# Optimization experiments

Measured on AMD Instinct MI355X. Metric: run time of the kernel, lower is better.

The kernel has to match this reference:

```python
import jax, jax.numpy as jnp
import numpy as np
import math

TIN = 4          # patch_size
NF = 128         # num_features
DM = 256         # d_model
NH = 8           # n_heads
HD = DM // NH    # head_dim = 32
FF = 1024        # ff_dim
NL = 4           # num_layers
MAXD = 64        # max_rel_dist -> L = 129


def _ln(x, g, b, eps):
    mu = jnp.mean(x, axis=-1, keepdims=True)
    var = jnp.mean(jnp.square(x - mu), axis=-1, keepdims=True)
    return (x - mu) * jax.lax.rsqrt(var + eps) * g + b


def setup_inputs() -> dict:
    key = jax.random.key(0)
    ks = jax.random.split(key, 24)
    s = 0.02
    d = {
        'x': jax.random.normal(ks[0], (2000, 16, NF), jnp.float32),
        'ln1_g': jnp.ones((TIN * NF,), jnp.float32),
        'ln1_b': jnp.zeros((TIN * NF,), jnp.float32),
        'proj_w': jax.random.normal(ks[1], (TIN * NF, DM), jnp.float32) * s,
        'proj_b': jnp.zeros((DM,), jnp.float32),
        'ln2_g': jnp.ones((DM,), jnp.float32),
        'ln2_b': jnp.zeros((DM,), jnp.float32),
        'rel_bias': jax.random.normal(ks[2], (NH, 2 * MAXD + 1), jnp.float32) * s,
        'ln_attn_g': jnp.ones((NL, DM), jnp.float32),
        'ln_attn_b': jnp.zeros((NL, DM), jnp.float32),
        'qkv_w': jax.random.normal(ks[3], (NL, DM, 3 * DM), jnp.float32) * s,
        'qkv_b': jnp.zeros((NL, 3 * DM), jnp.float32),
        'out_w': jax.random.normal(ks[4], (NL, DM, DM), jnp.float32) * s,
        'out_b': jnp.zeros((NL, DM), jnp.float32),
        'ln_ff_g': jnp.ones((NL, DM), jnp.float32),
        'ln_ff_b': jnp.zeros((NL, DM), jnp.float32),
        'ff1_w': jax.random.normal(ks[5], (NL, DM, FF), jnp.float32) * s,
        'ff1_b': jnp.zeros((NL, FF), jnp.float32),
        'ff2_w': jax.random.normal(ks[6], (NL, FF, DM), jnp.float32) * s,
        'ff2_b': jnp.zeros((NL, DM), jnp.float32),
        'fln_g': jnp.ones((DM,), jnp.float32),
        'fln_b': jnp.zeros((DM,), jnp.float32),
        'op_w': jax.random.normal(ks[7], (DM, NF), jnp.float32) * s,
        'op_b': jnp.zeros((NF,), jnp.float32),
    }
    return d


def reference(x, ln1_g, ln1_b, proj_w, proj_b, ln2_g, ln2_b, rel_bias,
              ln_attn_g, ln_attn_b, qkv_w, qkv_b, out_w, out_b,
              ln_ff_g, ln_ff_b, ff1_w, ff1_b, ff2_w, ff2_b,
              fln_g, fln_b, op_w, op_b):
    # ---- PatchEmbedding ----
    h = jnp.swapaxes(x, 0, 1)                 # [B, T, F]
    B, T, F = h.shape
    n_patch = T // TIN                        # 500 (== chunk_size, single chunk path)
    h = h[:, :n_patch * TIN, :].reshape(B, n_patch, TIN * F)
    h = _ln(h, ln1_g, ln1_b, 1e-6)
    h = h @ proj_w + proj_b
    h = _ln(h, ln2_g, ln2_b, 1e-6)            # [B, S, DM]
    S = n_patch

    # ---- relative position bias [H, S, S] ----
    pos = jnp.arange(S)
    rel = pos[None, :] - pos[:, None]
    idx = jnp.clip(rel, -MAXD, MAXD) + MAXD
    bias = rel_bias[:, idx]                   # [H, S, S]

    # ---- causal mask ----
    causal = jnp.triu(jnp.full((S, S), -jnp.inf, jnp.float32), k=1)
    scale = 1.0 / math.sqrt(HD)

    for l in range(NL):
        # attention block
        a = _ln(h, ln_attn_g[l], ln_attn_b[l], 1e-5)
        qkv = a @ qkv_w[l] + qkv_b[l]         # [B, S, 3*DM]
        q, k, v = jnp.split(qkv, 3, axis=-1)
        q = q.reshape(B, S, NH, HD)
        k = k.reshape(B, S, NH, HD)
        v = v.reshape(B, S, NH, HD)
        scores = jnp.einsum('bihd,bjhd->bhij', q, k) * scale
        scores = scores + bias[None] + causal
        attn = jax.nn.softmax(scores, axis=-1)
        o = jnp.einsum('bhij,bjhd->bihd', attn, v).reshape(B, S, DM)
        h = h + (o @ out_w[l] + out_b[l])
        # ffn block
        f = _ln(h, ln_ff_g[l], ln_ff_b[l], 1e-5)
        f = jax.nn.gelu(f @ ff1_w[l] + ff1_b[l], approximate=False)
        h = h + (f @ ff2_w[l] + ff2_b[l])

    h = _ln(h, fln_g, fln_b, 1e-5)
    h = h @ op_w + op_b                       # [B, S, NF]
    return jnp.swapaxes(h, 0, 1)              # [S, B, NF]
```

## Files before the change

### kernel.cpp

```cpp
#include <hip/hip_runtime.h>

#define TS 500
#define NB 16
#define NROW 8000
#define DMODEL 256
#define NHEAD 8
#define HDIM 32
#define FFD 1024

typedef __bf16 bf16x8 __attribute__((ext_vector_type(8)));
typedef __bf16 bf16x4 __attribute__((ext_vector_type(4)));
typedef float  f32x4  __attribute__((ext_vector_type(4)));
typedef float  f32x2  __attribute__((ext_vector_type(2)));

__device__ __forceinline__ float wred_sum(float v) {
    #pragma unroll
    for (int off = 32; off; off >>= 1) v += __shfl_xor(v, off, 64);
    return v;
}

__device__ __forceinline__ void pa_store(__bf16* __restrict__ PA, int KS,
                                         int grow, int col, float y) {
    int mt = grow >> 4, rl = grow & 15;
    size_t idx = ((size_t)(mt * KS + (col >> 5)) * 64 + ((col >> 3) & 3) * 16 + rl) * 8 + (col & 7);
// ... 33 lines not shown
    int k0 = ks * 32 + (lane >> 4) * 8;
    int col = nt * 16 + (lane & 15);
    const float* src = W + (size_t)l * wLS;
    bf16x8 v;
    #pragma unroll
    for (int j = 0; j < 8; j++) v[j] = (__bf16)src[(size_t)(k0 + j) * N + col];
    *(bf16x8*)(PB + (size_t)l * pLS + ((size_t)(nt * KS + ks) * 64 + lane) * 8) = v;
}

__global__ __launch_bounds__(256) void k_patchfused(
    const float* __restrict__ x, const float* __restrict__ g1, const float* __restrict__ b1,
    const __bf16* __restrict__ PBp, const float* __restrict__ bias,
    float* __restrict__ h,
    const float* __restrict__ gam, const float* __restrict__ bet,
    const float* __restrict__ gam2, const float* __restrict__ bet2,
    const __bf16* __restrict__ PBq0, const float* __restrict__ qb0,
    __bf16* __restrict__ qkvb)
{
    __shared__ __align__(16) __bf16 As[2][16][64][8];
    __shared__ float redS[4][32];
    __shared__ float redQ[4][32];
    int t = threadIdx.x, lane = t & 63, w = t >> 6;
    int row0 = blockIdx.x * 32;

    for (int rr = 0; rr < 8; rr++) {
        int lrow = w * 8 + rr;
        int row = row0 + lrow;
        int b = row / TS, pp = row - b * TS;
        int kb = lane * 8;
        const float* src = x + ((size_t)(pp * 4 + (kb >> 7)) * NB + b) * 128 + (kb & 127);
        float4 lo = *(const float4*)src;
        float4 hi = *(const float4*)(src + 4);
        float v[8] = {lo.x, lo.y, lo.z, lo.w, hi.x, hi.y, hi.z, hi.w};
        float sm_ = 0.f;
        #pragma unroll
        for (int j = 0; j < 8; j++) sm_ += v[j];
        sm_ = wred_sum(sm_);
        float mu = sm_ * (1.0f / 512.0f);
        float q = 0.f;
        #pragma unroll
        for (int j = 0; j < 8; j++) { float d = v[j] - mu; q += d * d; }
        q = wred_sum(q);
        float rs = rsqrtf(q * (1.0f / 512.0f) + 1e-6f);
        float4 gl = *(const float4*)(g1 + kb), gh = *(const float4*)(g1 + kb + 4);
        float4 bl = *(const float4*)(b1 + kb), bh = *(const float4*)(b1 + kb + 4);
        float gg[8] = {gl.x, gl.y, gl.z, gl.w, gh.x, gh.y, gh.z, gh.w};
        float bbv[8] = {bl.x, bl.y, bl.z, bl.w, bh.x, bh.y, bh.z, bh.w};
        bf16x8 yv;
        #pragma unroll
        for (int j = 0; j < 8; j++) yv[j] = (__bf16)((v[j] - mu) * rs * gg[j] + bbv[j]);
        *(bf16x8*)&As[lrow >> 4][lane >> 2][(lane & 3) * 16 + (lrow & 15)][0] = yv;
    }
    __syncthreads();

    const bf16x8* B8 = (const bf16x8*)PBp;
    f32x4 acc[2][4] = {};
    #pragma unroll 8
    for (int ks = 0; ks < 16; ks++) {
        bf16x8 a0 = *(const bf16x8*)&As[0][ks][lane][0];
        bf16x8 a1 = *(const bf16x8*)&As[1][ks][lane][0];
        #pragma unroll
        for (int n = 0; n < 4; n++) {
            bf16x8 b = B8[((size_t)(w * 4 + n) * 16 + ks) * 64 + lane];
            acc[0][n] = __builtin_amdgcn_mfma_f32_16x16x32_bf16(a0, b, acc[0][n], 0, 0, 0);
            acc[1][n] = __builtin_amdgcn_mfma_f32_16x16x32_bf16(a1, b, acc[1][n], 0, 0, 0);
        }
    }

    int g_ = lane >> 4, cl = lane & 15;
    int rbase = g_ * 4;
    float gamv[4], betv[4], gam2v[4], bet2v[4];
    #pragma unroll
    for (int n = 0; n < 4; n++) {
        int col = (w * 4 + n) * 16 + cl;
        float bv = bias[col];
        gamv[n] = gam[col]; betv[n] = bet[col];
        gam2v[n] = gam2[col]; bet2v[n] = bet2[col];
        #pragma unroll
        for (int m = 0; m < 2; m++)
            #pragma unroll
            for (int r = 0; r < 4; r++) acc[m][n][r] += bv;
    }
    float mu[2][4], rstd[2][4];
    {
        float ps[2][4];
        #pragma unroll
        for (int m = 0; m < 2; m++)
            #pragma unroll
            for (int r = 0; r < 4; r++) {
                float s2 = acc[m][0][r] + acc[m][1][r] + acc[m][2][r] + acc[m][3][r];
                #pragma unroll
                for (int off = 1; off < 16; off <<= 1) s2 += __shfl_xor(s2, off, 64);
                ps[m][r] = s2;
            }
        if (cl == 0)
            #pragma unroll
            for (int m = 0; m < 2; m++)
                #pragma unroll
                for (int r = 0; r < 4; r++) redS[w][m * 16 + rbase + r] = ps[m][r];
        __syncthreads();
        #pragma unroll
        for (int m = 0; m < 2; m++)
            #pragma unroll
            for (int r = 0; r < 4; r++) {
                int lr = m * 16 + rbase + r;
                mu[m][r] = (redS[0][lr] + redS[1][lr] + redS[2][lr] + redS[3][lr]) * (1.0f / 256.0f);
            }
        float pq[2][4];
        #pragma unroll
        for (int m = 0; m < 2; m++)
            #pragma unroll
            for (int r = 0; r < 4; r++) {
                float s2 = 0.f;
                #pragma unroll
                for (int n = 0; n < 4; n++) { float d = acc[m][n][r] - mu[m][r]; s2 += d * d; }
                #pragma unroll
                for (int off = 1; off < 16; off <<= 1) s2 += __shfl_xor(s2, off, 64);
                pq[m][r] = s2;
            }
        if (cl == 0)
            #pragma unroll
            for (int m = 0; m < 2; m++)
                #pragma unroll
                for (int r = 0; r < 4; r++) redQ[w][m * 16 + rbase + r] = pq[m][r];
        __syncthreads();
        #pragma unroll
        for (int m = 0; m < 2; m++)
            #pragma unroll
            for (int r = 0; r < 4; r++) {
                int lr = m * 16 + rbase + r;
                float var = (redQ[0][lr] + redQ[1][lr] + redQ[2][lr] + redQ[3][lr]) * (1.0f / 256.0f);
                rstd[m][r] = rsqrtf(var + 1e-6f);
            }
    }
    float ps2[2][4];
    #pragma unroll
    for (int m = 0; m < 2; m++) {
        int row = row0 + m * 16 + rbase;
        #pragma unroll
        for (int r = 0; r < 4; r++) {
            float s2 = 0.f;
            #pragma unroll
            for (int n = 0; n < 4; n++) {
                int col = (w * 4 + n) * 16 + cl;
                float y1 = (acc[m][n][r] - mu[m][r]) * rstd[m][r] * gamv[n] + betv[n];
                h[(size_t)(row + r) * 256 + col] = y1;
                s2 += y1;
            }
            #pragma unroll
            for (int off = 1; off < 16; off <<= 1) s2 += __shfl_xor(s2, off, 64);
            ps2[m][r] = s2;
        }
    }
    if (cl == 0)
        #pragma unroll
        for (int m = 0; m < 2; m++)
            #pragma unroll
            for (int r = 0; r < 4; r++) redS[w][m * 16 + rbase + r] = ps2[m][r];
    __syncthreads();
    float mu2[2][4], rstd2[2][4];
    #pragma unroll
    for (int m = 0; m < 2; m++)
        #pragma unroll
        for (int r = 0; r < 4; r++) {
            int lr = m * 16 + rbase + r;
            mu2[m][r] = (redS[0][lr] + redS[1][lr] + redS[2][lr] + redS[3][lr]) * (1.0f / 256.0f);
        }
    float pq2[2][4];
    #pragma unroll
    for (int m = 0; m < 2; m++)
        #pragma unroll
        for (int r = 0; r < 4; r++) {
            float s2 = 0.f;
            #pragma unroll
            for (int n = 0; n < 4; n++) {
                float y1 = (acc[m][n][r] - mu[m][r]) * rstd[m][r] * gamv[n] + betv[n];
                float d = y1 - mu2[m][r];
                s2 += d * d;
            }
            #pragma unroll
            for (int off = 1; off < 16; off <<= 1) s2 += __shfl_xor(s2, off, 64);
            pq2[m][r] = s2;
        }
    if (cl == 0)
        #pragma unroll
        for (int m = 0; m < 2; m++)
            #pragma unroll
            for (int r = 0; r < 4; r++) redQ[w][m * 16 + rbase + r] = pq2[m][r];
    __syncthreads();
    #pragma unroll
    for (int m = 0; m < 2; m++)
        #pragma unroll
        for (int r = 0; r < 4; r++) {
            int lr = m * 16 + rbase + r;
            float var = (redQ[0][lr] + redQ[1][lr] + redQ[2][lr] + redQ[3][lr]) * (1.0f / 256.0f);
            rstd2[m][r] = rsqrtf(var + 1e-5f);
        }
    __bf16* YA = &As[0][0][0][0];
    #pragma unroll
    for (int m = 0; m < 2; m++) {
        #pragma unroll
        for (int n = 0; n < 4; n++) {
            int col = (w * 4 + n) * 16 + cl;
            #pragma unroll
            for (int r = 0; r < 4; r++) {
                float y1 = (acc[m][n][r] - mu[m][r]) * rstd[m][r] * gamv[n] + betv[n];
                float y2 = (y1 - mu2[m][r]) * rstd2[m][r] * gam2v[n] + bet2v[n];
                ya_store(YA, m * 16 + rbase + r, col, y2);
            }
        }
    }
    __syncthreads();

    const bf16x8* YA8 = (const bf16x8*)YA;
    const bf16x8* B8q = (const bf16x8*)PBq0;
    for (int m = 0; m < 2; m++) {
        f32x4 acc2[12] = {};
        for (int ks = 0; ks < 8; ks++) {
            bf16x8 a = YA8[(m * 8 + ks) * 64 + lane];
            #pragma unroll
            for (int n = 0; n < 12; n++) {
                bf16x8 b = B8q[((size_t)(w * 12 + n) * 8 + ks) * 64 + lane];
                acc2[n] = __builtin_amdgcn_mfma_f32_16x16x32_bf16(a, b, acc2[n], 0, 0, 0);
            }
        }
        int row = row0 + m * 16 + rbase;
        #pragma unroll
        for (int n = 0; n < 12; n++) {
            int col = (w * 12 + n) * 16 + cl;
            float bv = qb0[col];
            #pragma unroll
            for (int r = 0; r < 4; r++)
                qkvb[(size_t)(row + r) * 768 + col] = (__bf16)(acc2[n][r] + bv);
        }
    }
}

template<int MODE>
__global__ __launch_bounds__(512) void k_layer(
    const __bf16* __restrict__ PAattn, const __bf16* __restrict__ PBo,
    const float* __restrict__ ob, float* __restrict__ h,
    const float* __restrict__ fg, const float* __restrict__ fb,
    const __bf16* __restrict__ PB1, const float* __restrict__ b1,
    const __bf16* __restrict__ PB2, const float* __restrict__ b2,
    const float* __restrict__ gam, const float* __restrict__ bet,
    const __bf16* __restrict__ PBn, const float* __restrict__ bn,
    __bf16* __restrict__ qkvb, float* __restrict__ outp)
{
    __shared__ __align__(16) __bf16 YA[8 * 64 * 8];
    __shared__ __align__(16) __bf16 F1T[1024][16];
    __shared__ float redS[8][16];
    __shared__ float redQ[8][16];
    int t = threadIdx.x, lane = t & 63, w = t >> 6;
    int mt = blockIdx.x;
    int g_ = lane >> 4, cl = lane & 15, rbase = g_ * 4;
    int row = mt * 16 + rbase;

    const bf16x8* A8 = (const bf16x8*)PAattn;
    const bf16x8* B8o = (const bf16x8*)PBo;
    const bf16x8* B81 = (const bf16x8*)PB1;
    const bf16x8* B82 = (const bf16x8*)PB2;

    f32x4 hv[2] = {};
    {
        f32x4 acc0[2] = {};
        #pragma unroll 8
        for (int ks = 0; ks < 8; ks++) {
            bf16x8 a = A8[((size_t)mt * 8 + ks) * 64 + lane];
            #pragma unroll
            for (int n = 0; n < 2; n++) {
                bf16x8 b = B8o[((size_t)(w * 2 + n) * 8 + ks) * 64 + lane];
                acc0[n] = __builtin_amdgcn_mfma_f32_16x16x32_bf16(a, b, acc0[n], 0, 0, 0);
            }
        }
        #pragma unroll
        for (int n = 0; n < 2; n++) {
            int col = (w * 2 + n) * 16 + cl;
            float bv = ob[col];
            #pragma unroll
            for (int r = 0; r < 4; r++)
                hv[n][r] = acc0[n][r] + bv + h[(size_t)(row + r) * 256 + col];
        }
    }
    {
        float mu[4], rstd[4];
        float ps[4];
        #pragma unroll
        for (int r = 0; r < 4; r++) {
            float s2 = hv[0][r] + hv[1][r];
            #pragma unroll
            for (int off = 1; off < 16; off <<= 1) s2 += __shfl_xor(s2, off, 64);
            ps[r] = s2;
        }
        if (cl == 0)
            #pragma unroll
            for (int r = 0; r < 4; r++) redS[w][rbase + r] = ps[r];
        __syncthreads();
        #pragma unroll
        for (int r = 0; r < 4; r++) {
            int lr = rbase + r;
            float s2 = 0.f;
            #pragma unroll
            for (int ww = 0; ww < 8; ww++) s2 += redS[ww][lr];
            mu[r] = s2 * (1.0f / 256.0f);
        }
        float pq[4];
        #pragma unroll
        for (int r = 0; r < 4; r++) {
            float s2 = 0.f;
            #pragma unroll
            for (int n = 0; n < 2; n++) { float d = hv[n][r] - mu[r]; s2 += d * d; }
            #pragma unroll
            for (int off = 1; off < 16; off <<= 1) s2 += __shfl_xor(s2, off, 64);
            pq[r] = s2;
        }
        if (cl == 0)
            #pragma unroll
            for (int r = 0; r < 4; r++) redQ[w][rbase + r] = pq[r];
        __syncthreads();
        #pragma unroll
        for (int r = 0; r < 4; r++) {
            int lr = rbase + r;
            float s2 = 0.f;
            #pragma unroll
            for (int ww = 0; ww < 8; ww++) s2 += redQ[ww][lr];
            rstd[r] = rsqrtf(s2 * (1.0f / 256.0f) + 1e-5f);
        }
        #pragma unroll
        for (int n = 0; n < 2; n++) {
            int col = (w * 2 + n) * 16 + cl;
            float gv = fg[col], bv = fb[col];
            #pragma unroll
            for (int r = 0; r < 4; r++) {
                float y = (hv[n][r] - mu[r]) * rstd[r] * gv + bv;
                ya_store(YA, rbase + r, col, y);
            }
        }
    }
    __syncthreads();

    const bf16x8* YA8 = (const bf16x8*)YA;
    {
        f32x4 acc1[8] = {};
        #pragma unroll 2
        for (int ks = 0; ks < 8; ks++) {
            bf16x8 a = YA8[ks * 64 + lane];
            #pragma unroll
            for (int n = 0; n < 8; n++) {
                bf16x8 b = B81[((size_t)(w * 8 + n) * 8 + ks) * 64 + lane];
                acc1[n] = __builtin_amdgcn_mfma_f32_16x16x32_bf16(a, b, acc1[n], 0, 0, 0);
            }
        }
        #pragma unroll
        for (int n = 0; n < 8; n++) {
            int col = (w * 8 + n) * 16 + cl;
            float bv = b1[col];
            bf16x4 pv;
            #pragma unroll
            for (int r = 0; r < 4; r++) {
                float xx = acc1[n][r] + bv;
                pv[r] = (__bf16)(0.5f * xx * (1.0f + erff(xx * 0.70710678118654752f)));
            }
            *(bf16x4*)&F1T[col][rbase] = pv;
        }
    }
    __syncthreads();

    f32x4 acc[2] = {};
    for (int kb = 0; kb < 8; kb++) {
        f32x2 lo[4], hi[4];
        #pragma unroll
        for (int q = 0; q < 4; q++) {
            unsigned ta = (unsigned)(uintptr_t)&F1T[(kb * 4 + q) * 32 + 8 * g_][0] + cl * 8;
            asm volatile("ds_read_b64_tr_b16 %0, %1" : "=v"(lo[q]) : "v"(ta) : "memory");
            asm volatile("ds_read_b64_tr_b16 %0, %1 offset:128" : "=v"(hi[q]) : "v"(ta) : "memory");
        }
        asm volatile("s_waitcnt lgkmcnt(0)" ::: "memory");
        __builtin_amdgcn_sched_barrier(0);
        #pragma unroll
        for (int q = 0; q < 4; q++) {
            int ks = kb * 4 + q;
            f32x4 pc = {lo[q][0], lo[q][1], hi[q][0], hi[q][1]};
            bf16x8 a = __builtin_bit_cast(bf16x8, pc);
            #pragma unroll
            for (int n = 0; n < 2; n++) {
                bf16x8 b = B82[((size_t)(w * 2 + n) * 32 + ks) * 64 + lane];
                acc[n] = __builtin_amdgcn_mfma_f32_16x16x32_bf16(a, b, acc[n], 0, 0, 0);
            }
        }
    }

    float gamv[2], betv[2];
    #pragma unroll
    for (int n = 0; n < 2; n++) {
        int col = (w * 2 + n) * 16 + cl;
        float bv = b2[col];
        gamv[n] = gam[col]; betv[n] = bet[col];
        #pragma unroll
        for (int r = 0; r < 4; r++) {
            float v = acc[n][r] + bv + hv[n][r];
            h[(size_t)(row + r) * 256 + col] = v;
            acc[n][r] = v;
        }
    }
    {
        float mu[4], rstd[4];
        float ps[4];
        #pragma unroll
        for (int r = 0; r < 4; r++) {
            float s2 = acc[0][r] + acc[1][r];
            #pragma unroll
            for (int off = 1; off < 16; off <<= 1) s2 += __shfl_xor(s2, off, 64);
            ps[r] = s2;
        }
        if (cl == 0)
            #pragma unroll
            for (int r = 0; r < 4; r++) redS[w][rbase + r] = ps[r];
        __syncthreads();
        #pragma unroll
        for (int r = 0; r < 4; r++) {
            int lr = rbase + r;
            float s2 = 0.f;
            #pragma unroll
            for (int ww = 0; ww < 8; ww++) s2 += redS[ww][lr];
            mu[r] = s2 * (1.0f / 256.0f);
        }
        float pq[4];
        #pragma unroll
        for (int r = 0; r < 4; r++) {
            float s2 = 0.f;
            #pragma unroll
            for (int n = 0; n < 2; n++) { float d = acc[n][r] - mu[r]; s2 += d * d; }
            #pragma unroll
            for (int off = 1; off < 16; off <<= 1) s2 += __shfl_xor(s2, off, 64);
            pq[r] = s2;
        }
        if (cl == 0)
            #pragma unroll
            for (int r = 0; r < 4; r++) redQ[w][rbase + r] = pq[r];
        __syncthreads();
        #pragma unroll
        for (int r = 0; r < 4; r++) {
            int lr = rbase + r;
            float s2 = 0.f;
            #pragma unroll
            for (int ww = 0; ww < 8; ww++) s2 += redQ[ww][lr];
            rstd[r] = rsqrtf(s2 * (1.0f / 256.0f) + 1e-5f);
        }
        #pragma unroll
        for (int n = 0; n < 2; n++) {
            int col = (w * 2 + n) * 16 + cl;
            #pragma unroll
            for (int r = 0; r < 4; r++) {
                float y = (acc[n][r] - mu[r]) * rstd[r] * gamv[n] + betv[n];
                ya_store(YA, rbase + r, col, y);
            }
        }
    }
    __syncthreads();

    const bf16x8* B8n = (const bf16x8*)PBn;
    if constexpr (MODE == 0) {
        f32x4 acc2[6] = {};
        for (int ks = 0; ks < 8; ks++) {
            bf16x8 a = YA8[ks * 64 + lane];
            #pragma unroll
            for (int n = 0; n < 6; n++) {
                bf16x8 b = B8n[((size_t)(w * 6 + n) * 8 + ks) * 64 + lane];
                acc2[n] = __builtin_amdgcn_mfma_f32_16x16x32_bf16(a, b, acc2[n], 0, 0, 0);
            }
        }
        #pragma unroll
        for (int n = 0; n < 6; n++) {
            int col = (w * 6 + n) * 16 + cl;
            float bv = bn[col];
            #pragma unroll
            for (int r = 0; r < 4; r++)
                qkvb[(size_t)(row + r) * 768 + col] = (__bf16)(acc2[n][r] + bv);
        }
    } else {
        f32x4 acc2 = {};
        #pragma unroll 4
        for (int ks = 0; ks < 8; ks++) {
            bf16x8 a = YA8[ks * 64 + lane];
            bf16x8 b = B8n[((size_t)w * 8 + ks) * 64 + lane];
            acc2 = __builtin_amdgcn_mfma_f32_16x16x32_bf16(a, b, acc2, 0, 0, 0);
        }
        int col = w * 16 + cl;
        float bv = bn[col];
        #pragma unroll
        for (int r = 0; r < 4; r++) {
            int grow = row + r;
            int bq = grow / TS, pp = grow - bq * TS;
            outp[((size_t)pp * NB + bq) * 128 + col] = acc2[r] + bv;
        }
    }
}

__global__ __launch_bounds__(512) void k_attn(
    const __bf16* __restrict__ qkv, const float* __restrict__ rel_bias,
    __bf16* __restrict__ PA)
{
    __shared__ __align__(16) __bf16 Kfr[4][64][8];
    __shared__ __align__(16) __bf16 Vpl[2][64][16];
    __shared__ __align__(16) __bf16 PT[8][64][16];
    __shared__ float bias_s[132];

    int bh = blockIdx.x;
    int pr = 3 - blockIdx.y;
    int b = bh >> 3, hh = bh & 7;
    int t = threadIdx.x, lane = t & 63, w = t >> 6;
    int wg = w & 3, grp = w >> 2;
    int qt = 2 * pr + 1 - grp;
    int q0 = qt * 64 + wg * 16;
    int c = lane & 15, g = lane >> 4;

    const __bf16* base = qkv + (size_t)b * TS * 768 + hh * 32;

    if (t < 129) bias_s[t] = rel_bias[hh * 129 + t];

    bf16x8 aq = {};
    {
        int qi = q0 + c;
        if (qi < TS) aq = *(const bf16x8*)(base + (size_t)qi * 768 + 8 * g);
    }

    float lpart[4] = {0.f, 0.f, 0.f, 0.f};
// ... 125 lines not shown
    const float* ln_ff_b  = (const float*)d_in[15];
    const float* ff1_w    = (const float*)d_in[16];
    const float* ff1_b    = (const float*)d_in[17];
    const float* ff2_w    = (const float*)d_in[18];
    const float* ff2_b    = (const float*)d_in[19];
    const float* fln_g    = (const float*)d_in[20];
    const float* fln_b    = (const float*)d_in[21];
    const float* op_w     = (const float*)d_in[22];
    const float* op_b     = (const float*)d_in[23];
    float* out = (float*)d_out;

    char* ws = (char*)d_ws;
    float*  h     = (float*)(ws);
    __bf16* qkvb  = (__bf16*)(ws + 8192000);
    __bf16* PA    = (__bf16*)(ws + 20480000);
    __bf16* PBq   = (__bf16*)(ws + 24576000);
    __bf16* PBo   = (__bf16*)(ws + 26148864);
    __bf16* PB1   = (__bf16*)(ws + 26673152);
    __bf16* PB2   = (__bf16*)(ws + 28770304);
    __bf16* PBp   = (__bf16*)(ws + 30867456);
    __bf16* PBop  = (__bf16*)(ws + 31129600);

    k_pack_all<<<1616, 256, 0, stream>>>(qkv_w, out_w, ff1_w, ff2_w, proj_w, op_w,
                                         PBq, PBo, PB1, PB2, PBp, PBop);

    k_patchfused<<<250, 256, 0, stream>>>(x, ln1_g, ln1_b, PBp, proj_b, h,
                                          ln2_g, ln2_b, ln_attn_g, ln_attn_b,
                                          PBq, qkv_b, qkvb);

    for (int l = 0; l < 4; l++) {
        dim3 ag(NB * NHEAD, 4);
        k_attn<<<ag, 512, 0, stream>>>(qkvb, rel_bias, PA);
        if (l < 3) {
            k_layer<0><<<500, 512, 0, stream>>>(PA, PBo + (size_t)l * 65536, out_b + l * 256,
                                                h, ln_ff_g + l * 256, ln_ff_b + l * 256,
                                                PB1 + (size_t)l * 262144, ff1_b + l * 1024,
                                                PB2 + (size_t)l * 262144, ff2_b + l * 256,
                                                ln_attn_g + (l + 1) * 256, ln_attn_b + (l + 1) * 256,
                                                PBq + (size_t)(l + 1) * 196608, qkv_b + (l + 1) * 768,
                                                qkvb, nullptr);
        } else {
            k_layer<1><<<500, 512, 0, stream>>>(PA, PBo + (size_t)l * 65536, out_b + l * 256,
                                                h, ln_ff_g + l * 256, ln_ff_b + l * 256,
                                                PB1 + (size_t)l * 262144, ff1_b + l * 1024,
                                                PB2 + (size_t)l * 262144, ff2_b + l * 256,
                                                fln_g, fln_b,
                                                PBop, op_b, nullptr, out);
        }
    }
}
```

Measured before the change: 283.7 us.

## Process two 16-row M tiles per layer block to reuse weight loads

Each k_layer block now handles 32 rows (two 16-row MFMA tiles) instead of 16, so every B-weight fragment loaded from global memory feeds two MFMAs. The FF1/FF2 stage is split into two halves of 512 columns so the transposed F1T buffer stays the same size in LDS. The grid is halved from 500 to 250 blocks. This cuts weight traffic per row but reduces parallelism below the CU count, raises register pressure, and adds extra barriers.

```diff
diff --git a/kernel.cpp b/kernel.cpp
--- a/kernel.cpp
+++ b/kernel.cpp
@@ -304,30 +304,31 @@
     const __bf16* __restrict__ PBn, const float* __restrict__ bn,
     __bf16* __restrict__ qkvb, float* __restrict__ outp)
 {
-    __shared__ __align__(16) __bf16 YA[8 * 64 * 8];
-    __shared__ __align__(16) __bf16 F1T[1024][16];
-    __shared__ float redS[8][16];
-    __shared__ float redQ[8][16];
+    __shared__ __align__(16) __bf16 YA[2 * 8 * 64 * 8];
+    __shared__ __align__(16) __bf16 F1T[2][512][16];
+    __shared__ float redS[8][32];
+    __shared__ float redQ[8][32];
     int t = threadIdx.x, lane = t & 63, w = t >> 6;
-    int mt = blockIdx.x;
+    int mt0 = blockIdx.x * 2;
     int g_ = lane >> 4, cl = lane & 15, rbase = g_ * 4;
-    int row = mt * 16 + rbase;
 
     const bf16x8* A8 = (const bf16x8*)PAattn;
     const bf16x8* B8o = (const bf16x8*)PBo;
     const bf16x8* B81 = (const bf16x8*)PB1;
     const bf16x8* B82 = (const bf16x8*)PB2;
 
-    f32x4 hv[2] = {};
+    f32x4 hv[2][2];
     {
-        f32x4 acc0[2] = {};
+        f32x4 acc0[2][2] = {};
         #pragma unroll 8
         for (int ks = 0; ks < 8; ks++) {
-            bf16x8 a = A8[((size_t)mt * 8 + ks) * 64 + lane];
+            bf16x8 a0 = A8[((size_t)mt0 * 8 + ks) * 64 + lane];
+            bf16x8 a1 = A8[((size_t)(mt0 + 1) * 8 + ks) * 64 + lane];
             #pragma unroll
             for (int n = 0; n < 2; n++) {
                 bf16x8 b = B8o[((size_t)(w * 2 + n) * 8 + ks) * 64 + lane];
-                acc0[n] = __builtin_amdgcn_mfma_f32_16x16x32_bf16(a, b, acc0[n], 0, 0, 0);
+                acc0[0][n] = __builtin_amdgcn_mfma_f32_16x16x32_bf16(a0, b, acc0[0][n], 0, 0, 0);
+                acc0[1][n] = __builtin_amdgcn_mfma_f32_16x16x32_bf16(a1, b, acc0[1][n], 0, 0, 0);
             }
         }
         #pragma unroll
@@ -335,116 +336,152 @@
             int col = (w * 2 + n) * 16 + cl;
             float bv = ob[col];
             #pragma unroll
-            for (int r = 0; r < 4; r++)
-                hv[n][r] = acc0[n][r] + bv + h[(size_t)(row + r) * 256 + col];
+            for (int m = 0; m < 2; m++) {
+                int row = (mt0 + m) * 16 + rbase;
+                #pragma unroll
+                for (int r = 0; r < 4; r++)
+                    hv[m][n][r] = acc0[m][n][r] + bv + h[(size_t)(row + r) * 256 + col];
+            }
         }
     }
     {
-        float mu[4], rstd[4];
-        float ps[4];
-        #pragma unroll
-        for (int r = 0; r < 4; r++) {
-            float s2 = hv[0][r] + hv[1][r];
-            #pragma unroll
-            for (int off = 1; off < 16; off <<= 1) s2 += __shfl_xor(s2, off, 64);
-            ps[r] = s2;
-        }
+        float mu[2][4], rstd[2][4];
+        float ps[2][4];
+        #pragma unroll
+        for (int m = 0; m < 2; m++)
+            #pragma unroll
+            for (int r = 0; r < 4; r++) {
+                float s2 = hv[m][0][r] + hv[m][1][r];
+                #pragma unroll
+                for (int off = 1; off < 16; off <<= 1) s2 += __shfl_xor(s2, off, 64);
+                ps[m][r] = s2;
+            }
         if (cl == 0)
             #pragma unroll
-            for (int r = 0; r < 4; r++) redS[w][rbase + r] = ps[r];
-        __syncthreads();
-        #pragma unroll
-        for (int r = 0; r < 4; r++) {
-            int lr = rbase + r;
-            float s2 = 0.f;
-            #pragma unroll
-            for (int ww = 0; ww < 8; ww++) s2 += redS[ww][lr];
-            mu[r] = s2 * (1.0f / 256.0f);
-        }
-        float pq[4];
-        #pragma unroll
-        for (int r = 0; r < 4; r++) {
-            float s2 = 0.f;
-            #pragma unroll
-            for (int n = 0; n < 2; n++) { float d = hv[n][r] - mu[r]; s2 += d * d; }
-            #pragma unroll
-            for (int off = 1; off < 16; off <<= 1) s2 += __shfl_xor(s2, off, 64);
-            pq[r] = s2;
-        }
+            for (int m = 0; m < 2; m++)
+                #pragma unroll
+                for (int r = 0; r < 4; r++) redS[w][m * 16 + rbase + r] = ps[m][r];
+        __syncthreads();
+        #pragma unroll
+        for (int m = 0; m < 2; m++)
+            #pragma unroll
+            for (int r = 0; r < 4; r++) {
+                int lr = m * 16 + rbase + r;
+                float s2 = 0.f;
+                #pragma unroll
+                for (int ww = 0; ww < 8; ww++) s2 += redS[ww][lr];
+                mu[m][r] = s2 * (1.0f / 256.0f);
+            }
+        float pq[2][4];
+        #pragma unroll
+        for (int m = 0; m < 2; m++)
+            #pragma unroll
+            for (int r = 0; r < 4; r++) {
+                float s2 = 0.f;
+                #pragma unroll
+                for (int n = 0; n < 2; n++) { float d = hv[m][n][r] - mu[m][r]; s2 += d * d; }
+                #pragma unroll
+                for (int off = 1; off < 16; off <<= 1) s2 += __shfl_xor(s2, off, 64);
+                pq[m][r] = s2;
+            }
         if (cl == 0)
             #pragma unroll
-            for (int r = 0; r < 4; r++) redQ[w][rbase + r] = pq[r];
-        __syncthreads();
-        #pragma unroll
-        for (int r = 0; r < 4; r++) {
-            int lr = rbase + r;
-            float s2 = 0.f;
-            #pragma unroll
-            for (int ww = 0; ww < 8; ww++) s2 += redQ[ww][lr];
-            rstd[r] = rsqrtf(s2 * (1.0f / 256.0f) + 1e-5f);
-        }
+            for (int m = 0; m < 2; m++)
+                #pragma unroll
+                for (int r = 0; r < 4; r++) redQ[w][m * 16 + rbase + r] = pq[m][r];
+        __syncthreads();
+        #pragma unroll
+        for (int m = 0; m < 2; m++)
+            #pragma unroll
+            for (int r = 0; r < 4; r++) {
+                int lr = m * 16 + rbase + r;
+                float s2 = 0.f;
+                #pragma unroll
+                for (int ww = 0; ww < 8; ww++) s2 += redQ[ww][lr];
+                rstd[m][r] = rsqrtf(s2 * (1.0f / 256.0f) + 1e-5f);
+            }
         #pragma unroll
         for (int n = 0; n < 2; n++) {
             int col = (w * 2 + n) * 16 + cl;
             float gv = fg[col], bv = fb[col];
             #pragma unroll
-            for (int r = 0; r < 4; r++) {
-                float y = (hv[n][r] - mu[r]) * rstd[r] * gv + bv;
-                ya_store(YA, rbase + r, col, y);
-            }
+            for (int m = 0; m < 2; m++)
+                #pragma unroll
+                for (int r = 0; r < 4; r++) {
+                    float y = (hv[m][n][r] - mu[m][r]) * rstd[m][r] * gv + bv;
+                    ya_store(YA, m * 16 + rbase + r, col, y);
+                }
         }
     }
     __syncthreads();
 
     const bf16x8* YA8 = (const bf16x8*)YA;
-    {
-        f32x4 acc1[8] = {};
-        #pragma unroll 2
-        for (int ks = 0; ks < 8; ks++) {
-            bf16x8 a = YA8[ks * 64 + lane];
-            #pragma unroll
-            for (int n = 0; n < 8; n++) {
-                bf16x8 b = B81[((size_t)(w * 8 + n) * 8 + ks) * 64 + lane];
-                acc1[n] = __builtin_amdgcn_mfma_f32_16x16x32_bf16(a, b, acc1[n], 0, 0, 0);
-            }
-        }
-        #pragma unroll
-        for (int n = 0; n < 8; n++) {
-            int col = (w * 8 + n) * 16 + cl;
-            float bv = b1[col];
-            bf16x4 pv;
-            #pragma unroll
-            for (int r = 0; r < 4; r++) {
-                float xx = acc1[n][r] + bv;
-                pv[r] = (__bf16)(0.5f * xx * (1.0f + erff(xx * 0.70710678118654752f)));
-            }
-            *(bf16x4*)&F1T[col][rbase] = pv;
-        }
-    }
-    __syncthreads();
-
-    f32x4 acc[2] = {};
-    for (int kb = 0; kb < 8; kb++) {
-        f32x2 lo[4], hi[4];
-        #pragma unroll
-        for (int q = 0; q < 4; q++) {
-            unsigned ta = (unsigned)(uintptr_t)&F1T[(kb * 4 + q) * 32 + 8 * g_][0] + cl * 8;
-            asm volatile("ds_read_b64_tr_b16 %0, %1" : "=v"(lo[q]) : "v"(ta) : "memory");
-            asm volatile("ds_read_b64_tr_b16 %0, %1 offset:128" : "=v"(hi[q]) : "v"(ta) : "memory");
-        }
-        asm volatile("s_waitcnt lgkmcnt(0)" ::: "memory");
-        __builtin_amdgcn_sched_barrier(0);
-        #pragma unroll
-        for (int q = 0; q < 4; q++) {
-            int ks = kb * 4 + q;
-            f32x4 pc = {lo[q][0], lo[q][1], hi[q][0], hi[q][1]};
-            bf16x8 a = __builtin_bit_cast(bf16x8, pc);
-            #pragma unroll
-            for (int n = 0; n < 2; n++) {
-                bf16x8 b = B82[((size_t)(w * 2 + n) * 32 + ks) * 64 + lane];
-                acc[n] = __builtin_amdgcn_mfma_f32_16x16x32_bf16(a, b, acc[n], 0, 0, 0);
-            }
-        }
+    f32x4 acc[2][2] = {};
+    #pragma unroll
+    for (int hf = 0; hf < 2; hf++) {
+        {
+            f32x4 acc1[2][4] = {};
+            #pragma unroll 2
+            for (int ks = 0; ks < 8; ks++) {
+                bf16x8 a0 = YA8[ks * 64 + lane];
+                bf16x8 a1 = YA8[(8 + ks) * 64 + lane];
+                #pragma unroll
+                for (int n = 0; n < 4; n++) {
+                    int nt = hf * 32 + w * 4 + n;
+                    bf16x8 b = B81[((size_t)nt * 8 + ks) * 64 + lane];
+                    acc1[0][n] = __builtin_amdgcn_mfma_f32_16x16x32_bf16(a0, b, acc1[0][n], 0, 0, 0);
+                    acc1[1][n] = __builtin_amdgcn_mfma_f32_16x16x32_bf16(a1, b, acc1[1][n], 0, 0, 0);
+                }
+            }
+            #pragma unroll
+            for (int n = 0; n < 4; n++) {
+                int colh = (w * 4 + n) * 16 + cl;
+                float bv = b1[hf * 512 + colh];
+                #pragma unroll
+                for (int m = 0; m < 2; m++) {
+                    bf16x4 pv;
+                    #pragma unroll
+                    for (int r = 0; r < 4; r++) {
+                        float xx = acc1[m][n][r] + bv;
+                        pv[r] = (__bf16)(0.5f * xx * (1.0f + erff(xx * 0.70710678118654752f)));
+                    }
+                    *(bf16x4*)&F1T[m][colh][rbase] = pv;
+                }
+            }
+        }
+        __syncthreads();
+
+        for (int kb = 0; kb < 4; kb++) {
+            f32x2 lo[2][4], hi[2][4];
+            #pragma unroll
+            for (int q = 0; q < 4; q++) {
+                #pragma unroll
+                for (int m = 0; m < 2; m++) {
+                    unsigned ta = (unsigned)(uintptr_t)&F1T[m][(kb * 4 + q) * 32 + 8 * g_][0] + cl * 8;
+                    asm volatile("ds_read_b64_tr_b16 %0, %1" : "=v"(lo[m][q]) : "v"(ta) : "memory");
+                    asm volatile("ds_read_b64_tr_b16 %0, %1 offset:128" : "=v"(hi[m][q]) : "v"(ta) : "memory");
+                }
+            }
+            asm volatile("s_waitcnt lgkmcnt(0)" ::: "memory");
+            __builtin_amdgcn_sched_barrier(0);
+            #pragma unroll
+            for (int q = 0; q < 4; q++) {
+                int ks = hf * 16 + kb * 4 + q;
+                bf16x8 a[2];
+                #pragma unroll
+                for (int m = 0; m < 2; m++) {
+                    f32x4 pc = {lo[m][q][0], lo[m][q][1], hi[m][q][0], hi[m][q][1]};
+                    a[m] = __builtin_bit_cast(bf16x8, pc);
+                }
+                #pragma unroll
+                for (int n = 0; n < 2; n++) {
+                    bf16x8 b = B82[((size_t)(w * 2 + n) * 32 + ks) * 64 + lane];
+                    acc[0][n] = __builtin_amdgcn_mfma_f32_16x16x32_bf16(a[0], b, acc[0][n], 0, 0, 0);
+                    acc[1][n] = __builtin_amdgcn_mfma_f32_16x16x32_bf16(a[1], b, acc[1][n], 0, 0, 0);
+                }
+            }
+        }
+        __syncthreads();
     }
 
     float gamv[2], betv[2];
@@ -454,77 +491,97 @@
         float bv = b2[col];
         gamv[n] = gam[col]; betv[n] = bet[col];
         #pragma unroll
-        for (int r = 0; r < 4; r++) {
-            float v = acc[n][r] + bv + hv[n][r];
-            h[(size_t)(row + r) * 256 + col] = v;
-            acc[n][r] = v;
+        for (int m = 0; m < 2; m++) {
+            int row = (mt0 + m) * 16 + rbase;
+            #pragma unroll
+            for (int r = 0; r < 4; r++) {
+                float v = acc[m][n][r] + bv + hv[m][n][r];
+                h[(size_t)(row + r) * 256 + col] = v;
+                acc[m][n][r] = v;
+            }
         }
     }
     {
-        float mu[4], rstd[4];
-        float ps[4];
-        #pragma unroll
-        for (int r = 0; r < 4; r++) {
-            float s2 = acc[0][r] + acc[1][r];
-            #pragma unroll
-            for (int off = 1; off < 16; off <<= 1) s2 += __shfl_xor(s2, off, 64);
-            ps[r] = s2;
-        }
+        float mu[2][4], rstd[2][4];
+        float ps[2][4];
+        #pragma unroll
+        for (int m = 0; m < 2; m++)
+            #pragma unroll
+            for (int r = 0; r < 4; r++) {
+                float s2 = acc[m][0][r] + acc[m][1][r];
+                #pragma unroll
+                for (int off = 1; off < 16; off <<= 1) s2 += __shfl_xor(s2, off, 64);
+                ps[m][r] = s2;
+            }
         if (cl == 0)
             #pragma unroll
-            for (int r = 0; r < 4; r++) redS[w][rbase + r] = ps[r];
-        __syncthreads();
-        #pragma unroll
-        for (int r = 0; r < 4; r++) {
-            int lr = rbase + r;
-            float s2 = 0.f;
-            #pragma unroll
-            for (int ww = 0; ww < 8; ww++) s2 += redS[ww][lr];
-            mu[r] = s2 * (1.0f / 256.0f);
-        }
-        float pq[4];
-        #pragma unroll
-        for (int r = 0; r < 4; r++) {
-            float s2 = 0.f;
-            #pragma unroll
-            for (int n = 0; n < 2; n++) { float d = acc[n][r] - mu[r]; s2 += d * d; }
-            #pragma unroll
-            for (int off = 1; off < 16; off <<= 1) s2 += __shfl_xor(s2, off, 64);
-            pq[r] = s2;
-        }
+            for (int m = 0; m < 2; m++)
+                #pragma unroll
+                for (int r = 0; r < 4; r++) redS[w][m * 16 + rbase + r] = ps[m][r];
+        __syncthreads();
+        #pragma unroll
+        for (int m = 0; m < 2; m++)
+            #pragma unroll
+            for (int r = 0; r < 4; r++) {
+                int lr = m * 16 + rbase + r;
+                float s2 = 0.f;
+                #pragma unroll
+                for (int ww = 0; ww < 8; ww++) s2 += redS[ww][lr];
+                mu[m][r] = s2 * (1.0f / 256.0f);
+            }
+        float pq[2][4];
+        #pragma unroll
+        for (int m = 0; m < 2; m++)
+            #pragma unroll
+            for (int r = 0; r < 4; r++) {
+                float s2 = 0.f;
+                #pragma unroll
+                for (int n = 0; n < 2; n++) { float d = acc[m][n][r] - mu[m][r]; s2 += d * d; }
+                #pragma unroll
+                for (int off = 1; off < 16; off <<= 1) s2 += __shfl_xor(s2, off, 64);
+                pq[m][r] = s2;
+            }
         if (cl == 0)
             #pragma unroll
-            for (int r = 0; r < 4; r++) redQ[w][rbase + r] = pq[r];
-        __syncthreads();
-        #pragma unroll
-        for (int r = 0; r < 4; r++) {
-            int lr = rbase + r;
-            float s2 = 0.f;
-            #pragma unroll
-            for (int ww = 0; ww < 8; ww++) s2 += redQ[ww][lr];
-            rstd[r] = rsqrtf(s2 * (1.0f / 256.0f) + 1e-5f);
-        }
+            for (int m = 0; m < 2; m++)
+                #pragma unroll
+                for (int r = 0; r < 4; r++) redQ[w][m * 16 + rbase + r] = pq[m][r];
+        __syncthreads();
+        #pragma unroll
+        for (int m = 0; m < 2; m++)
+            #pragma unroll
+            for (int r = 0; r < 4; r++) {
+                int lr = m * 16 + rbase + r;
+                float s2 = 0.f;
+                #pragma unroll
+                for (int ww = 0; ww < 8; ww++) s2 += redQ[ww][lr];
+                rstd[m][r] = rsqrtf(s2 * (1.0f / 256.0f) + 1e-5f);
+            }
         #pragma unroll
         for (int n = 0; n < 2; n++) {
             int col = (w * 2 + n) * 16 + cl;
             #pragma unroll
-            for (int r = 0; r < 4; r++) {
-                float y = (acc[n][r] - mu[r]) * rstd[r] * gamv[n] + betv[n];
-                ya_store(YA, rbase + r, col, y);
-            }
+            for (int m = 0; m < 2; m++)
+                #pragma unroll
+                for (int r = 0; r < 4; r++) {
+                    float y = (acc[m][n][r] - mu[m][r]) * rstd[m][r] * gamv[n] + betv[n];
+                    ya_store(YA, m * 16 + rbase + r, col, y);
+                }
         }
     }
     __syncthreads();
 
     const bf16x8* B8n = (const bf16x8*)PBn;
     if constexpr (MODE == 0) {
-        f32x4 acc2[6] = {};
+        f32x4 acc2[2][6] = {};
         for (int ks = 0; ks < 8; ks++) {
-            bf16x8 a = YA8[ks * 64 + lane];
+            bf16x8 a0 = YA8[ks * 64 + lane];
+            bf16x8 a1 = YA8[(8 + ks) * 64 + lane];
             #pragma unroll
             for (int n = 0; n < 6; n++) {
                 bf16x8 b = B8n[((size_t)(w * 6 + n) * 8 + ks) * 64 + lane];
-                acc2[n] = __builtin_amdgcn_mfma_f32_16x16x32_bf16(a, b, acc2[n], 0, 0, 0);
+                acc2[0][n] = __builtin_amdgcn_mfma_f32_16x16x32_bf16(a0, b, acc2[0][n], 0, 0, 0);
+                acc2[1][n] = __builtin_amdgcn_mfma_f32_16x16x32_bf16(a1, b, acc2[1][n], 0, 0, 0);
             }
         }
         #pragma unroll
@@ -532,24 +589,34 @@
             int col = (w * 6 + n) * 16 + cl;
             float bv = bn[col];
             #pragma unroll
-            for (int r = 0; r < 4; r++)
-                qkvb[(size_t)(row + r) * 768 + col] = (__bf16)(acc2[n][r] + bv);
+            for (int m = 0; m < 2; m++) {
+                int row = (mt0 + m) * 16 + rbase;
+                #pragma unroll
+                for (int r = 0; r < 4; r++)
+                    qkvb[(size_t)(row + r) * 768 + col] = (__bf16)(acc2[m][n][r] + bv);
+            }
         }
     } else {
-        f32x4 acc2 = {};
+        f32x4 acc2[2] = {};
         #pragma unroll 4
         for (int ks = 0; ks < 8; ks++) {
-            bf16x8 a = YA8[ks * 64 + lane];
+            bf16x8 a0 = YA8[ks * 64 + lane];
+            bf16x8 a1 = YA8[(8 + ks) * 64 + lane];
             bf16x8 b = B8n[((size_t)w * 8 + ks) * 64 + lane];
-            acc2 = __builtin_amdgcn_mfma_f32_16x16x32_bf16(a, b, acc2, 0, 0, 0);
+            acc2[0] = __builtin_amdgcn_mfma_f32_16x16x32_bf16(a0, b, acc2[0], 0, 0, 0);
+            acc2[1] = __builtin_amdgcn_mfma_f32_16x16x32_bf16(a1, b, acc2[1], 0, 0, 0);
         }
         int col = w * 16 + cl;
         float bv = bn[col];
         #pragma unroll
-        for (int r = 0; r < 4; r++) {
-            int grow = row + r;
-            int bq = grow / TS, pp = grow - bq * TS;
-            outp[((size_t)pp * NB + bq) * 128 + col] = acc2[r] + bv;
+        for (int m = 0; m < 2; m++) {
+            int row = (mt0 + m) * 16 + rbase;
+            #pragma unroll
+            for (int r = 0; r < 4; r++) {
+                int grow = row + r;
+                int bq = grow / TS, pp = grow - bq * TS;
+                outp[((size_t)pp * NB + bq) * 128 + col] = acc2[m][r] + bv;
+            }
         }
     }
 }
@@ -741,7 +808,7 @@
         dim3 ag(NB * NHEAD, 4);
         k_attn<<<ag, 512, 0, stream>>>(qkvb, rel_bias, PA);
         if (l < 3) {
-            k_layer<0><<<500, 512, 0, stream>>>(PA, PBo + (size_t)l * 65536, out_b + l * 256,
+            k_layer<0><<<250, 512, 0, stream>>>(PA, PBo + (size_t)l * 65536, out_b + l * 256,
                                                 h, ln_ff_g + l * 256, ln_ff_b + l * 256,
                                                 PB1 + (size_t)l * 262144, ff1_b + l * 1024,
                                                 PB2 + (size_t)l * 262144, ff2_b + l * 256,
@@ -749,7 +816,7 @@
                                                 PBq + (size_t)(l + 1) * 196608, qkv_b + (l + 1) * 768,
                                                 qkvb, nullptr);
         } else {
-            k_layer<1><<<500, 512, 0, stream>>>(PA, PBo + (size_t)l * 65536, out_b + l * 256,
+            k_layer<1><<<250, 512, 0, stream>>>(PA, PBo + (size_t)l * 65536, out_b + l * 256,
                                                 h, ln_ff_g + l * 256, ln_ff_b + l * 256,
                                                 PB1 + (size_t)l * 262144, ff1_b + l * 1024,
                                                 PB2 + (size_t)l * 262144, ff2_b + l * 256,
```

After: 311.7 us. 9.9% more time.

## Fuse LayerNorm mean/variance reductions and prefetch first weight tiles across barriers

Applied to the files above, without the earlier changes.

LayerNorm statistics now come from a single pass that accumulates sum and sum of squares together, with variance taken as E[x^2]-mu^2. This halves the shuffle reductions and removes one __syncthreads per LayerNorm in the embed and layer kernels. The first K-slice of the FF1, FF2 and next-layer weight fragments is also prefetched into registers before the LayerNorm barriers, with sched_barrier fences so the global loads overlap the reductions. The one-pass variance is less numerically stable, and the prefetch buffers raise register pressure.

```diff
diff --git a/kernel.cpp b/kernel.cpp
--- a/kernel.cpp
+++ b/kernel.cpp
@@ -89,16 +89,13 @@
         float4 lo = *(const float4*)src;
         float4 hi = *(const float4*)(src + 4);
         float v[8] = {lo.x, lo.y, lo.z, lo.w, hi.x, hi.y, hi.z, hi.w};
-        float sm_ = 0.f;
-        #pragma unroll
-        for (int j = 0; j < 8; j++) sm_ += v[j];
+        float sm_ = 0.f, qq = 0.f;
+        #pragma unroll
+        for (int j = 0; j < 8; j++) { sm_ += v[j]; qq += v[j] * v[j]; }
         sm_ = wred_sum(sm_);
+        qq = wred_sum(qq);
         float mu = sm_ * (1.0f / 512.0f);
-        float q = 0.f;
-        #pragma unroll
-        for (int j = 0; j < 8; j++) { float d = v[j] - mu; q += d * d; }
-        q = wred_sum(q);
-        float rs = rsqrtf(q * (1.0f / 512.0f) + 1e-6f);
+        float rs = rsqrtf(qq * (1.0f / 512.0f) - mu * mu + 1e-6f);
         float4 gl = *(const float4*)(g1 + kb), gh = *(const float4*)(g1 + kb + 4);
         float4 bl = *(const float4*)(b1 + kb), bh = *(const float4*)(b1 + kb + 4);
         float gg[8] = {gl.x, gl.y, gl.z, gl.w, gh.x, gh.y, gh.z, gh.w};
@@ -140,118 +137,85 @@
     }
     float mu[2][4], rstd[2][4];
     {
-        float ps[2][4];
+        float ps[2][4], pq[2][4];
         #pragma unroll
         for (int m = 0; m < 2; m++)
             #pragma unroll
             for (int r = 0; r < 4; r++) {
                 float s2 = acc[m][0][r] + acc[m][1][r] + acc[m][2][r] + acc[m][3][r];
+                float q2 = acc[m][0][r] * acc[m][0][r] + acc[m][1][r] * acc[m][1][r]
+                         + acc[m][2][r] * acc[m][2][r] + acc[m][3][r] * acc[m][3][r];
                 #pragma unroll
-                for (int off = 1; off < 16; off <<= 1) s2 += __shfl_xor(s2, off, 64);
-                ps[m][r] = s2;
+                for (int off = 1; off < 16; off <<= 1) {
+                    s2 += __shfl_xor(s2, off, 64);
+                    q2 += __shfl_xor(q2, off, 64);
+                }
+                ps[m][r] = s2; pq[m][r] = q2;
             }
         if (cl == 0)
             #pragma unroll
             for (int m = 0; m < 2; m++)
                 #pragma unroll
-                for (int r = 0; r < 4; r++) redS[w][m * 16 + rbase + r] = ps[m][r];
+                for (int r = 0; r < 4; r++) {
+                    redS[w][m * 16 + rbase + r] = ps[m][r];
+                    redQ[w][m * 16 + rbase + r] = pq[m][r];
+                }
         __syncthreads();
         #pragma unroll
         for (int m = 0; m < 2; m++)
             #pragma unroll
             for (int r = 0; r < 4; r++) {
                 int lr = m * 16 + rbase + r;
-                mu[m][r] = (redS[0][lr] + redS[1][lr] + redS[2][lr] + redS[3][lr]) * (1.0f / 256.0f);
-            }
-        float pq[2][4];
-        #pragma unroll
-        for (int m = 0; m < 2; m++)
+                float s2 = (redS[0][lr] + redS[1][lr] + redS[2][lr] + redS[3][lr]) * (1.0f / 256.0f);
+                float q2 = (redQ[0][lr] + redQ[1][lr] + redQ[2][lr] + redQ[3][lr]) * (1.0f / 256.0f);
+                mu[m][r] = s2;
+                rstd[m][r] = rsqrtf(q2 - s2 * s2 + 1e-6f);
+            }
+    }
+    __syncthreads();
+    {
+        float ps2[2][4], pq2[2][4];
+        #pragma unroll
+        for (int m = 0; m < 2; m++) {
+            int row = row0 + m * 16 + rbase;
             #pragma unroll
             for (int r = 0; r < 4; r++) {
-                float s2 = 0.f;
+                float s2 = 0.f, q2 = 0.f;
                 #pragma unroll
-                for (int n = 0; n < 4; n++) { float d = acc[m][n][r] - mu[m][r]; s2 += d * d; }
+                for (int n = 0; n < 4; n++) {
+                    int col = (w * 4 + n) * 16 + cl;
+                    float y1 = (acc[m][n][r] - mu[m][r]) * rstd[m][r] * gamv[n] + betv[n];
+                    h[(size_t)(row + r) * 256 + col] = y1;
+                    s2 += y1; q2 += y1 * y1;
+                }
                 #pragma unroll
-                for (int off = 1; off < 16; off <<= 1) s2 += __shfl_xor(s2, off, 64);
-                pq[m][r] = s2;
-            }
+                for (int off = 1; off < 16; off <<= 1) {
+                    s2 += __shfl_xor(s2, off, 64);
+                    q2 += __shfl_xor(q2, off, 64);
+                }
+                ps2[m][r] = s2; pq2[m][r] = q2;
+            }
+        }
         if (cl == 0)
             #pragma unroll
             for (int m = 0; m < 2; m++)
                 #pragma unroll
-                for (int r = 0; r < 4; r++) redQ[w][m * 16 + rbase + r] = pq[m][r];
+                for (int r = 0; r < 4; r++) {
+                    redS[w][m * 16 + rbase + r] = ps2[m][r];
+                    redQ[w][m * 16 + rbase + r] = pq2[m][r];
+                }
         __syncthreads();
-        #pragma unroll
-        for (int m = 0; m < 2; m++)
-            #pragma unroll
-            for (int r = 0; r < 4; r++) {
-                int lr = m * 16 + rbase + r;
-                float var = (redQ[0][lr] + redQ[1][lr] + redQ[2][lr] + redQ[3][lr]) * (1.0f / 256.0f);
-                rstd[m][r] = rsqrtf(var + 1e-6f);
-            }
-    }
-    float ps2[2][4];
-    #pragma unroll
-    for (int m = 0; m < 2; m++) {
-        int row = row0 + m * 16 + rbase;
-        #pragma unroll
-        for (int r = 0; r < 4; r++) {
-            float s2 = 0.f;
-            #pragma unroll
-            for (int n = 0; n < 4; n++) {
-                int col = (w * 4 + n) * 16 + cl;
-                float y1 = (acc[m][n][r] - mu[m][r]) * rstd[m][r] * gamv[n] + betv[n];
-                h[(size_t)(row + r) * 256 + col] = y1;
-                s2 += y1;
-            }
-            #pragma unroll
-            for (int off = 1; off < 16; off <<= 1) s2 += __shfl_xor(s2, off, 64);
-            ps2[m][r] = s2;
-        }
-    }
-    if (cl == 0)
-        #pragma unroll
-        for (int m = 0; m < 2; m++)
-            #pragma unroll
-            for (int r = 0; r < 4; r++) redS[w][m * 16 + rbase + r] = ps2[m][r];
-    __syncthreads();
+    }
     float mu2[2][4], rstd2[2][4];
     #pragma unroll
     for (int m = 0; m < 2; m++)
         #pragma unroll
         for (int r = 0; r < 4; r++) {
             int lr = m * 16 + rbase + r;
-            mu2[m][r] = (redS[0][lr] + redS[1][lr] + redS[2][lr] + redS[3][lr]) * (1.0f / 256.0f);
-        }
-    float pq2[2][4];
-    #pragma unroll
-    for (int m = 0; m < 2; m++)
-        #pragma unroll
-        for (int r = 0; r < 4; r++) {
-            float s2 = 0.f;
-            #pragma unroll
-            for (int n = 0; n < 4; n++) {
-                float y1 = (acc[m][n][r] - mu[m][r]) * rstd[m][r] * gamv[n] + betv[n];
-                float d = y1 - mu2[m][r];
-                s2 += d * d;
-            }
-            #pragma unroll
-            for (int off = 1; off < 16; off <<= 1) s2 += __shfl_xor(s2, off, 64);
-            pq2[m][r] = s2;
-        }
-    if (cl == 0)
-        #pragma unroll
-        for (int m = 0; m < 2; m++)
-            #pragma unroll
-            for (int r = 0; r < 4; r++) redQ[w][m * 16 + rbase + r] = pq2[m][r];
-    __syncthreads();
-    #pragma unroll
-    for (int m = 0; m < 2; m++)
-        #pragma unroll
-        for (int r = 0; r < 4; r++) {
-            int lr = m * 16 + rbase + r;
-            float var = (redQ[0][lr] + redQ[1][lr] + redQ[2][lr] + redQ[3][lr]) * (1.0f / 256.0f);
-            rstd2[m][r] = rsqrtf(var + 1e-5f);
+            float s2 = (redS[0][lr] + redS[1][lr] + redS[2][lr] + redS[3][lr]) * (1.0f / 256.0f);
+            float q2 = (redQ[0][lr] + redQ[1][lr] + redQ[2][lr] + redQ[3][lr]) * (1.0f / 256.0f);
+            mu2[m][r] = s2;
+            rstd2[m][r] = rsqrtf(q2 - s2 * s2 + 1e-5f);
         }
     __bf16* YA = &As[0][0][0][0];
     #pragma unroll
@@ -339,49 +303,39 @@
                 hv[n][r] = acc0[n][r] + bv + h[(size_t)(row + r) * 256 + col];
         }
     }
+
+    bf16x8 pfA[8];
+    #pragma unroll
+    for (int n = 0; n < 8; n++)
+        pfA[n] = B81[((size_t)(w * 8 + n) * 8) * 64 + lane];
+
     {
         float mu[4], rstd[4];
-        float ps[4];
+        float ps[4], pq[4];
         #pragma unroll
         for (int r = 0; r < 4; r++) {
             float s2 = hv[0][r] + hv[1][r];
-            #pragma unroll
-            for (int off = 1; off < 16; off <<= 1) s2 += __shfl_xor(s2, off, 64);
-            ps[r] = s2;
+            float q2 = hv[0][r] * hv[0][r] + hv[1][r] * hv[1][r];
+            #pragma unroll
+            for (int off = 1; off < 16; off <<= 1) {
+                s2 += __shfl_xor(s2, off, 64);
+                q2 += __shfl_xor(q2, off, 64);
+            }
+            ps[r] = s2; pq[r] = q2;
         }
         if (cl == 0)
             #pragma unroll
-            for (int r = 0; r < 4; r++) redS[w][rbase + r] = ps[r];
+            for (int r = 0; r < 4; r++) { redS[w][rbase + r] = ps[r]; redQ[w][rbase + r] = pq[r]; }
         __syncthreads();
         #pragma unroll
         for (int r = 0; r < 4; r++) {
             int lr = rbase + r;
-            float s2 = 0.f;
-            #pragma unroll
-            for (int ww = 0; ww < 8; ww++) s2 += redS[ww][lr];
-            mu[r] = s2 * (1.0f / 256.0f);
-        }
-        float pq[4];
-        #pragma unroll
-        for (int r = 0; r < 4; r++) {
-            float s2 = 0.f;
-            #pragma unroll
-            for (int n = 0; n < 2; n++) { float d = hv[n][r] - mu[r]; s2 += d * d; }
-            #pragma unroll
-            for (int off = 1; off < 16; off <<= 1) s2 += __shfl_xor(s2, off, 64);
-            pq[r] = s2;
-        }
-        if (cl == 0)
-            #pragma unroll
-            for (int r = 0; r < 4; r++) redQ[w][rbase + r] = pq[r];
-        __syncthreads();
-        #pragma unroll
-        for (int r = 0; r < 4; r++) {
-            int lr = rbase + r;
-            float s2 = 0.f;
-            #pragma unroll
-            for (int ww = 0; ww < 8; ww++) s2 += redQ[ww][lr];
-            rstd[r] = rsqrtf(s2 * (1.0f / 256.0f) + 1e-5f);
+            float s2 = 0.f, q2 = 0.f;
+            #pragma unroll
+            for (int ww = 0; ww < 8; ww++) { s2 += redS[ww][lr]; q2 += redQ[ww][lr]; }
+            s2 *= (1.0f / 256.0f); q2 *= (1.0f / 256.0f);
+            mu[r] = s2;
+            rstd[r] = rsqrtf(q2 - s2 * s2 + 1e-5f);
         }
         #pragma unroll
         for (int n = 0; n < 2; n++) {
@@ -394,13 +348,21 @@
             }
         }
     }
+    __builtin_amdgcn_sched_barrier(0);
     __syncthreads();
 
     const bf16x8* YA8 = (const bf16x8*)YA;
+    bf16x8 pfB[8];
     {
         f32x4 acc1[8] = {};
+        {
+            bf16x8 a = YA8[lane];
+            #pragma unroll
+            for (int n = 0; n < 8; n++)
+                acc1[n] = __builtin_amdgcn_mfma_f32_16x16x32_bf16(a, pfA[n], acc1[n], 0, 0, 0);
+        }
         #pragma unroll 2
-        for (int ks = 0; ks < 8; ks++) {
+        for (int ks = 1; ks < 8; ks++) {
             bf16x8 a = YA8[ks * 64 + lane];
             #pragma unroll
             for (int n = 0; n < 8; n++) {
@@ -408,6 +370,12 @@
                 acc1[n] = __builtin_amdgcn_mfma_f32_16x16x32_bf16(a, b, acc1[n], 0, 0, 0);
             }
         }
+        #pragma unroll
+        for (int q = 0; q < 4; q++)
+            #pragma unroll
+            for (int n = 0; n < 2; n++)
+                pfB[q * 2 + n] = B82[((size_t)(w * 2 + n) * 32 + q) * 64 + lane];
+
         #pragma unroll
         for (int n = 0; n < 8; n++) {
             int col = (w * 8 + n) * 16 + cl;
@@ -421,6 +389,7 @@
             *(bf16x4*)&F1T[col][rbase] = pv;
         }
     }
+    __builtin_amdgcn_sched_barrier(0);
     __syncthreads();
 
     f32x4 acc[2] = {};
@@ -441,7 +410,8 @@
             bf16x8 a = __builtin_bit_cast(bf16x8, pc);
             #pragma unroll
             for (int n = 0; n < 2; n++) {
-                bf16x8 b = B82[((size_t)(w * 2 + n) * 32 + ks) * 64 + lane];
+                bf16x8 b = (kb == 0) ? pfB[q * 2 + n]
+                                     : B82[((size_t)(w * 2 + n) * 32 + ks) * 64 + lane];
                 acc[n] = __builtin_amdgcn_mfma_f32_16x16x32_bf16(a, b, acc[n], 0, 0, 0);
             }
         }
@@ -460,49 +430,44 @@
             acc[n][r] = v;
         }
     }
+
+    const bf16x8* B8n = (const bf16x8*)PBn;
+    bf16x8 pfT[6];
+    if constexpr (MODE == 0) {
+        #pragma unroll
+        for (int n = 0; n < 6; n++)
+            pfT[n] = B8n[((size_t)(w * 6 + n) * 8) * 64 + lane];
+    } else {
+        pfT[0] = B8n[((size_t)w * 8) * 64 + lane];
+    }
+
     {
         float mu[4], rstd[4];
-        float ps[4];
+        float ps[4], pq[4];
         #pragma unroll
         for (int r = 0; r < 4; r++) {
             float s2 = acc[0][r] + acc[1][r];
-            #pragma unroll
-            for (int off = 1; off < 16; off <<= 1) s2 += __shfl_xor(s2, off, 64);
-            ps[r] = s2;
+            float q2 = acc[0][r] * acc[0][r] + acc[1][r] * acc[1][r];
+            #pragma unroll
+            for (int off = 1; off < 16; off <<= 1) {
+                s2 += __shfl_xor(s2, off, 64);
+                q2 += __shfl_xor(q2, off, 64);
+            }
+            ps[r] = s2; pq[r] = q2;
         }
         if (cl == 0)
             #pragma unroll
-            for (int r = 0; r < 4; r++) redS[w][rbase + r] = ps[r];
+            for (int r = 0; r < 4; r++) { redS[w][rbase + r] = ps[r]; redQ[w][rbase + r] = pq[r]; }
         __syncthreads();
         #pragma unroll
         for (int r = 0; r < 4; r++) {
             int lr = rbase + r;
-            float s2 = 0.f;
-            #pragma unroll
-            for (int ww = 0; ww < 8; ww++) s2 += redS[ww][lr];
-            mu[r] = s2 * (1.0f / 256.0f);
-        }
-        float pq[4];
-        #pragma unroll
-        for (int r = 0; r < 4; r++) {
-            float s2 = 0.f;
-            #pragma unroll
-            for (int n = 0; n < 2; n++) { float d = acc[n][r] - mu[r]; s2 += d * d; }
-            #pragma unroll
-            for (int off = 1; off < 16; off <<= 1) s2 += __shfl_xor(s2, off, 64);
-            pq[r] = s2;
-        }
-        if (cl == 0)
-            #pragma unroll
-            for (int r = 0; r < 4; r++) redQ[w][rbase + r] = pq[r];
-        __syncthreads();
-        #pragma unroll
-        for (int r = 0; r < 4; r++) {
-            int lr = rbase + r;
-            float s2 = 0.f;
-            #pragma unroll
-            for (int ww = 0; ww < 8; ww++) s2 += redQ[ww][lr];
-            rstd[r] = rsqrtf(s2 * (1.0f / 256.0f) + 1e-5f);
+            float s2 = 0.f, q2 = 0.f;
+            #pragma unroll
+            for (int ww = 0; ww < 8; ww++) { s2 += redS[ww][lr]; q2 += redQ[ww][lr]; }
+            s2 *= (1.0f / 256.0f); q2 *= (1.0f / 256.0f);
+            mu[r] = s2;
+            rstd[r] = rsqrtf(q2 - s2 * s2 + 1e-5f);
         }
         #pragma unroll
         for (int n = 0; n < 2; n++) {
@@ -514,12 +479,18 @@
             }
         }
     }
+    __builtin_amdgcn_sched_barrier(0);
     __syncthreads();
 
-    const bf16x8* B8n = (const bf16x8*)PBn;
     if constexpr (MODE == 0) {
         f32x4 acc2[6] = {};
-        for (int ks = 0; ks < 8; ks++) {
+        {
+            bf16x8 a = YA8[lane];
+            #pragma unroll
+            for (int n = 0; n < 6; n++)
+                acc2[n] = __builtin_amdgcn_mfma_f32_16x16x32_bf16(a, pfT[n], acc2[n], 0, 0, 0);
+        }
+        for (int ks = 1; ks < 8; ks++) {
             bf16x8 a = YA8[ks * 64 + lane];
             #pragma unroll
             for (int n = 0; n < 6; n++) {
@@ -537,8 +508,12 @@
         }
     } else {
         f32x4 acc2 = {};
+        {
+            bf16x8 a = YA8[lane];
+            acc2 = __builtin_amdgcn_mfma_f32_16x16x32_bf16(a, pfT[0], acc2, 0, 0, 0);
+        }
         #pragma unroll 4
-        for (int ks = 0; ks < 8; ks++) {
+        for (int ks = 1; ks < 8; ks++) {
             bf16x8 a = YA8[ks * 64 + lane];
             bf16x8 b = B8n[((size_t)w * 8 + ks) * 64 + lane];
             acc2 = __builtin_amdgcn_mfma_f32_16x16x32_bf16(a, b, acc2, 0, 0, 0);
```

Result: slower. 350.2 us (+23.4%).
